# Kernel optimization log

Hardware: AMD Instinct MI355X
Metric: run time of the kernel (lower is better)

## Reference

```python
import jax, jax.numpy as jnp
import numpy as np

N_ITER = 50  # bisection iterations (matches entmax_bisect default)


def entmax_bisect(x, alpha):
    """alpha-entmax via bisection along axis=1. x: [B, L, 1], alpha: [1] (>1)."""
    a_m1 = alpha - 1.0
    inv = 1.0 / a_m1
    xs = x * a_m1
    d = x.shape[1]
    max_val = jnp.max(xs, axis=1, keepdims=True)
    tau_lo = max_val - 1.0
    tau_hi = max_val - (1.0 / d) ** a_m1
    f_lo = jnp.sum(jnp.maximum(xs - tau_lo, 0.0) ** inv, axis=1, keepdims=True) - 1.0

    def body(i, carry):
        tau_lo, dm = carry
        dm = dm * 0.5
        tau_m = tau_lo + dm
        f_m = jnp.sum(jnp.maximum(xs - tau_m, 0.0) ** inv, axis=1, keepdims=True) - 1.0
        tau_lo = jnp.where(f_m * f_lo >= 0.0, tau_m, tau_lo)
        return (tau_lo, dm)

    tau_lo, dm = jax.lax.fori_loop(0, N_ITER, body, (tau_lo, tau_hi - tau_lo))
    p = jnp.maximum(xs - (tau_lo + 0.5 * dm), 0.0) ** inv
    return p / jnp.sum(p, axis=1, keepdims=True)


def setup_inputs() -> dict:
    key = jax.random.key(0)
    ks = jax.random.split(key, 8)
    B, L, E2, D = 256, 512, 512, 256  # E2 = emb_size * 2
    C_target = jax.random.normal(ks[0], (B, E2), jnp.float32)
    C = jax.random.normal(ks[1], (B, L, E2), jnp.float32)
    X = jax.random.normal(ks[2], (B, E2, D), jnp.float32)
    alpha = jnp.array([1.5], jnp.float32)  # entmax-1.5
    mask = jax.random.randint(ks[3], (B, L), 0, 2, jnp.int32).at[:, 0].set(1)
    s = 1.0 / np.sqrt(E2)
    Wg1 = jax.random.uniform(ks[4], (E2, E2), jnp.float32, -s, s)
    Wg2 = jax.random.uniform(ks[5], (E2, E2), jnp.float32, -s, s)
    Wg0 = jax.random.uniform(ks[6], (E2, 1), jnp.float32, -s, s)
    bias_alpha = jax.random.normal(ks[7], (E2,), jnp.float32) * 0.02
    return dict(C_target=C_target, C=C, X=X, alpha=alpha, mask=mask,
                Wg1=Wg1, Wg2=Wg2, Wg0=Wg0, bias_alpha=bias_alpha)


def reference(C_target, C, X, alpha, mask, Wg1, Wg2, Wg0, bias_alpha):
    q = C_target[:, None, :]                               # [B, 1, 2E]
    h = jax.nn.relu(C @ Wg1 + q @ Wg2 + bias_alpha)        # [B, L, 2E]
    score = h @ Wg0                                        # [B, L, 1]
    score = jnp.where(mask[..., None] == 0, -1e30, score)  # mask -> -inf
    p = entmax_bisect(score, alpha)                        # sparse attn over L
    attn = jnp.swapaxes(p, 1, 2) @ C                       # [B, 1, 2E]
    out = jnp.sum(attn @ X, axis=1)                        # [B, D]
    return out
```

## Files before the change

kernel.cpp:

```cpp
#include <hip/hip_runtime.h>
#include <hip/hip_bf16.h>

typedef __bf16 bf16_t;
typedef bf16_t bf16x8 __attribute__((ext_vector_type(8)));
typedef float f32x4 __attribute__((ext_vector_type(4)));

__global__ void k_wg1t(const float* __restrict__ Wg1, bf16_t* __restrict__ Wg1T) {
    __shared__ float tile[32][33];
    const int k0 = blockIdx.x * 32;
    const int e0 = blockIdx.y * 32;
    const int tx = threadIdx.x;
    const int ty = threadIdx.y;
    #pragma unroll
    for (int i = 0; i < 32; i += 8)
        tile[ty + i][tx] = Wg1[(k0 + ty + i) * 512 + e0 + tx];
    __syncthreads();
    #pragma unroll
    for (int i = 0; i < 32; i += 8)
        Wg1T[(e0 + ty + i) * 512 + k0 + tx] = (bf16_t)tile[tx][ty + i];
}

__global__ __launch_bounds__(256) void k_gate(const float* __restrict__ Ct,
                                              const float* __restrict__ Wg2,
                                              const float* __restrict__ bias,
                                              float* __restrict__ g) {
    __shared__ float q[512];
    const int b = blockIdx.x;
    const int t = threadIdx.x;
    q[t]       = Ct[b * 512 + t];
    q[t + 256] = Ct[b * 512 + t + 256];
    __syncthreads();
    const int e = (blockIdx.y << 8) + t;
    float acc = bias[e];
    #pragma unroll 8
    for (int k = 0; k < 512; ++k)
        acc = fmaf(q[k], Wg2[k * 512 + e], acc);
    g[b * 512 + e] = acc;
}

__global__ __launch_bounds__(256, 2) void k_score(const float* __restrict__ C,
                                                  const bf16_t* __restrict__ Wg1T,
                                                  const float* __restrict__ g,
                                                  const float* __restrict__ Wg0,
                                                  const int* __restrict__ mask,
                                                  float* __restrict__ score) {
    __shared__ bf16_t As[64 * 32];
    __shared__ bf16_t Bs[512 * 32];
    __shared__ float  sred[4][64];

    const int t    = threadIdx.x;
    const int lane = t & 63;
    const int wave = t >> 6;
    const int quad = lane >> 4;
    const int l15  = lane & 15;
    const int row0 = blockIdx.x * 64;
    const int b    = row0 >> 9;

    f32x4 acc[4][8] = {};

    for (int kc = 0; kc < 512; kc += 32) {
        __syncthreads();
        #pragma unroll
        for (int i = 0; i < 8; ++i) {
            const int f  = i * 256 + t;
            const int r  = f >> 2;
            const int c8 = (f & 3) << 3;
            __builtin_amdgcn_global_load_lds(
                (const __attribute__((address_space(1))) void*)(Wg1T + r * 512 + kc + c8),
                (__attribute__((address_space(3))) void*)(Bs + f * 8), 16, 0, 0);
        }
        #pragma unroll
        for (int i = 0; i < 2; ++i) {
            const int f  = i * 256 + t;
            const int r  = f >> 3;
            const int c4 = (f & 7) << 2;
            const float4 v = *reinterpret_cast<const float4*>(
                &C[(size_t)(row0 + r) * 512 + kc + c4]);
            union { bf16_t h[4]; uint2 u; } pk;
            pk.h[0] = (bf16_t)v.x; pk.h[1] = (bf16_t)v.y;
            pk.h[2] = (bf16_t)v.z; pk.h[3] = (bf16_t)v.w;
            *reinterpret_cast<uint2*>(&As[r * 32 + c4]) = pk.u;
        }
        __syncthreads();
        bf16x8 afr[4], bfr[8];
        #pragma unroll
        for (int mi = 0; mi < 4; ++mi)
            afr[mi] = *reinterpret_cast<const bf16x8*>(
                &As[(mi * 16 + l15) * 32 + quad * 8]);
        #pragma unroll
        for (int ni = 0; ni < 8; ++ni)
            bfr[ni] = *reinterpret_cast<const bf16x8*>(
                &Bs[(wave * 128 + ni * 16 + l15) * 32 + quad * 8]);
        #pragma unroll
        for (int mi = 0; mi < 4; ++mi)
            #pragma unroll
            for (int ni = 0; ni < 8; ++ni)
                acc[mi][ni] = __builtin_amdgcn_mfma_f32_16x16x32_bf16(
                    afr[mi], bfr[ni], acc[mi][ni], 0, 0, 0);
    }

    float rsum[16];
    #pragma unroll
    for (int i = 0; i < 16; ++i) rsum[i] = 0.f;
    #pragma unroll
    for (int ni = 0; ni < 8; ++ni) {
        const int n  = wave * 128 + ni * 16 + l15;
        const float gv = g[(b << 9) + n];
        const float w0 = Wg0[n];
        #pragma unroll
        for (int mi = 0; mi < 4; ++mi)
            #pragma unroll
            for (int r = 0; r < 4; ++r) {
                float u = fmaxf(acc[mi][ni][r] + gv, 0.f);
                rsum[mi * 4 + r] = fmaf(u, w0, rsum[mi * 4 + r]);
            }
    }
    #pragma unroll
    for (int i = 0; i < 16; ++i) {
        float v = rsum[i];
        v += __shfl_xor(v, 1);
        v += __shfl_xor(v, 2);
        v += __shfl_xor(v, 4);
        v += __shfl_xor(v, 8);
        rsum[i] = v;
    }
    if (l15 == 0) {
        #pragma unroll
        for (int mi = 0; mi < 4; ++mi)
            #pragma unroll
            for (int r = 0; r < 4; ++r)
                sred[wave][mi * 16 + quad * 4 + r] = rsum[mi * 4 + r];
    }
    __syncthreads();
    if (t < 64) {
        const float sc = sred[0][t] + sred[1][t] + sred[2][t] + sred[3][t];
        const int grow = row0 + t;
        score[grow] = (mask[grow] == 0) ? -1e30f : sc;
    }
}

__global__ __launch_bounds__(256) void k_entmax(const float* __restrict__ score,
                                                const float* __restrict__ alpha,
                                                float* __restrict__ p) {
    const int wave = threadIdx.x >> 6;
    const int lane = threadIdx.x & 63;
    const int b    = (blockIdx.x << 2) + wave;
    const float am1 = alpha[0] - 1.0f;
    const float inv = 1.0f / am1;
    const bool  sq  = fabsf(inv - 2.0f) < 1e-6f;

    const float* sb = score + (b << 9);
    float x[8];
    {
        const float4 v0 = *reinterpret_cast<const float4*>(sb + lane * 8);
        const float4 v1 = *reinterpret_cast<const float4*>(sb + lane * 8 + 4);
        x[0] = v0.x * am1; x[1] = v0.y * am1; x[2] = v0.z * am1; x[3] = v0.w * am1;
        x[4] = v1.x * am1; x[5] = v1.y * am1; x[6] = v1.z * am1; x[7] = v1.w * am1;
    }
    float m = x[0];
    #pragma unroll
    for (int j = 1; j < 8; ++j) m = fmaxf(m, x[j]);
    #pragma unroll
    for (int s = 1; s < 64; s <<= 1) m = fmaxf(m, __shfl_xor(m, s));

    float tau_lo = m - 1.0f;
    float dm = (m - powf(1.0f / 512.0f, am1)) - tau_lo;

    float f_lo;
    {
        float s = 0.f;
        #pragma unroll
        for (int j = 0; j < 8; ++j) {
            const float u = fmaxf(x[j] - tau_lo, 0.f);
            s += sq ? u * u : powf(u, inv);
        }
        #pragma unroll
        for (int sh = 1; sh < 64; sh <<= 1) s += __shfl_xor(s, sh);
        f_lo = s - 1.0f;
    }
    for (int it = 0; it < 50; ++it) {
        dm *= 0.5f;
        const float tau_m = tau_lo + dm;
        float s = 0.f;
        #pragma unroll
        for (int j = 0; j < 8; ++j) {
            const float u = fmaxf(x[j] - tau_m, 0.f);
            s += sq ? u * u : powf(u, inv);
        }
        #pragma unroll
        for (int sh = 1; sh < 64; sh <<= 1) s += __shfl_xor(s, sh);
        if ((s - 1.0f) * f_lo >= 0.f) tau_lo = tau_m;
    }
    const float tau = tau_lo + 0.5f * dm;
    float pj[8];
    float Z = 0.f;
    #pragma unroll
    for (int j = 0; j < 8; ++j) {
        const float u = fmaxf(x[j] - tau, 0.f);
        pj[j] = sq ? u * u : powf(u, inv);
        Z += pj[j];
    }
    #pragma unroll
    for (int sh = 1; sh < 64; sh <<= 1) Z += __shfl_xor(Z, sh);
    const float rz = 1.0f / Z;
    float4 o0, o1;
    o0.x = pj[0] * rz; o0.y = pj[1] * rz; o0.z = pj[2] * rz; o0.w = pj[3] * rz;
    o1.x = pj[4] * rz; o1.y = pj[5] * rz; o1.z = pj[6] * rz; o1.w = pj[7] * rz;
    *reinterpret_cast<float4*>(p + (b << 9) + lane * 8)     = o0;
    *reinterpret_cast<float4*>(p + (b << 9) + lane * 8 + 4) = o1;
}

__global__ __launch_bounds__(256) void k_attn(const float* __restrict__ p,
                                              const float* __restrict__ C,
                                              float* __restrict__ part) {
    __shared__ float pv_s[128];
    const int b  = blockIdx.x;
    const int ch = blockIdx.y;
    const int t  = threadIdx.x;
    const float* Cb = C + (size_t)b * 512 * 512 + (size_t)ch * 128 * 512;
    const float* pb = p + (b << 9) + (ch << 7);
    if (t < 128) pv_s[t] = pb[t];
    __syncthreads();
    float a0 = 0.f, a1 = 0.f;
    for (int l = 0; l < 128; ++l) {
        const float pv = pv_s[l];
        if (pv != 0.f) {
            a0 = fmaf(pv, Cb[(size_t)l * 512 + t], a0);
            a1 = fmaf(pv, Cb[(size_t)l * 512 + t + 256], a1);
        }
    }
    float* pp = part + (size_t)((b << 2) + ch) * 512;
    pp[t]       = a0;
    pp[t + 256] = a1;
}

__global__ __launch_bounds__(256) void k_out(const float* __restrict__ part,
                                             const float* __restrict__ X,
                                             float* __restrict__ out) {
    __shared__ float as_[128];
    const int b  = blockIdx.x;
    const int ec = blockIdx.y;
    const int t  = threadIdx.x;
    if (t < 128) {
        const int e = (ec << 7) + t;
        const float* pp = part + (size_t)(b << 2) * 512;
        as_[t] = pp[e] + pp[512 + e] + pp[1024 + e] + pp[1536 + e];
    }
    __syncthreads();
    const float* Xb = X + (size_t)b * 512 * 256 + (size_t)(ec << 7) * 256;
    float acc = 0.f;
    #pragma unroll 4
    for (int e = 0; e < 128; ++e)
        acc = fmaf(as_[e], Xb[e * 256 + t], acc);
    atomicAdd(&out[(b << 8) + t], acc);
}

extern "C" void kernel_launch(void* const* d_in, const int* in_sizes, int n_in,
                              void* d_out, int out_size, void* d_ws, size_t ws_size,
                              hipStream_t stream) {
    const float* C_target = (const float*)d_in[0];
    const float* C        = (const float*)d_in[1];
    const float* X        = (const float*)d_in[2];
    const float* alpha    = (const float*)d_in[3];
    const int*   mask     = (const int*)  d_in[4];
    const float* Wg1      = (const float*)d_in[5];
    const float* Wg2      = (const float*)d_in[6];
    const float* Wg0      = (const float*)d_in[7];
    const float* bias     = (const float*)d_in[8];
    float* out = (float*)d_out;

    char* ws = (char*)d_ws;
    bf16_t* wg1t  = (bf16_t*)(ws);
    float*  g     = (float*)(ws + (512u << 10));
    float*  score = (float*)(ws + (1024u << 10));
    float*  p     = (float*)(ws + (1536u << 10));
    float*  part  = (float*)(ws + (2048u << 10));

    k_wg1t  <<<dim3(16, 16), dim3(32, 8), 0, stream>>>(Wg1, wg1t);
    k_gate  <<<dim3(256, 2), 256, 0, stream>>>(C_target, Wg2, bias, g);
    k_score <<<2048, 256, 0, stream>>>(C, wg1t, g, Wg0, mask, score);
    k_entmax<<<64, 256, 0, stream>>>(score, alpha, p);
    k_attn  <<<dim3(256, 4), 256, 0, stream>>>(p, C, part);
    hipMemsetAsync(d_out, 0, (size_t)out_size * sizeof(float), stream);
    k_out   <<<dim3(256, 4), 256, 0, stream>>>(part, X, out);
}
```

Baseline: 595.5 us.

## Restructure score GEMM: stage C in swizzled LDS, stream Wg1T via registers

The score kernel now converts a 64x256 chunk of C to bf16 in swizzled LDS (two phases over K) instead of looping over 16 small K-chunks. Wg1T is no longer staged through LDS: each wave loads its B fragments straight from global/L2 with register double-buffering. This cuts the number of block barriers and avoids LDS bank conflicts, at the cost of more register pressure and repeated global reads of Wg1T across blocks. Separately, entmax launches one 64-thread block per batch row instead of four rows per block, and the k_out loop unroll is raised to 8.

```diff
diff --git a/kernel.cpp b/kernel.cpp
--- a/kernel.cpp
+++ b/kernel.cpp
@@ -44,8 +44,7 @@
                                                   const float* __restrict__ Wg0,
                                                   const int* __restrict__ mask,
                                                   float* __restrict__ score) {
-    __shared__ bf16_t As[64 * 32];
-    __shared__ bf16_t Bs[512 * 32];
+    __shared__ bf16_t As[64 * 256];
     __shared__ float  sred[4][64];
 
     const int t    = threadIdx.x;
@@ -55,48 +54,61 @@
     const int l15  = lane & 15;
     const int row0 = blockIdx.x * 64;
     const int b    = row0 >> 9;
+    const int nb   = wave * 128;
 
     f32x4 acc[4][8] = {};
 
-    for (int kc = 0; kc < 512; kc += 32) {
+    #pragma unroll
+    for (int ph = 0; ph < 2; ++ph) {
+        const int k0 = ph << 8;
         __syncthreads();
         #pragma unroll
-        for (int i = 0; i < 8; ++i) {
-            const int f  = i * 256 + t;
-            const int r  = f >> 2;
-            const int c8 = (f & 3) << 3;
-            __builtin_amdgcn_global_load_lds(
-                (const __attribute__((address_space(1))) void*)(Wg1T + r * 512 + kc + c8),
-                (__attribute__((address_space(3))) void*)(Bs + f * 8), 16, 0, 0);
-        }
-        #pragma unroll
-        for (int i = 0; i < 2; ++i) {
-            const int f  = i * 256 + t;
-            const int r  = f >> 3;
-            const int c4 = (f & 7) << 2;
+        for (int i = 0; i < 16; ++i) {
+            const int s  = i * 256 + t;
+            const int r  = s >> 6;
+            const int c4 = (s & 63) << 2;
             const float4 v = *reinterpret_cast<const float4*>(
-                &C[(size_t)(row0 + r) * 512 + kc + c4]);
+                &C[(size_t)(row0 + r) * 512 + k0 + c4]);
             union { bf16_t h[4]; uint2 u; } pk;
             pk.h[0] = (bf16_t)v.x; pk.h[1] = (bf16_t)v.y;
             pk.h[2] = (bf16_t)v.z; pk.h[3] = (bf16_t)v.w;
-            *reinterpret_cast<uint2*>(&As[r * 32 + c4]) = pk.u;
+            const int col = ((((c4 >> 3) ^ (r & 31)) << 3) | (c4 & 7));
+            *reinterpret_cast<uint2*>(&As[r * 256 + col]) = pk.u;
         }
         __syncthreads();
-        bf16x8 afr[4], bfr[8];
-        #pragma unroll
-        for (int mi = 0; mi < 4; ++mi)
-            afr[mi] = *reinterpret_cast<const bf16x8*>(
-                &As[(mi * 16 + l15) * 32 + quad * 8]);
+        bf16x8 bcur[8];
         #pragma unroll
         for (int ni = 0; ni < 8; ++ni)
-            bfr[ni] = *reinterpret_cast<const bf16x8*>(
-                &Bs[(wave * 128 + ni * 16 + l15) * 32 + quad * 8]);
-        #pragma unroll
-        for (int mi = 0; mi < 4; ++mi)
-            #pragma unroll
-            for (int ni = 0; ni < 8; ++ni)
-                acc[mi][ni] = __builtin_amdgcn_mfma_f32_16x16x32_bf16(
-                    afr[mi], bfr[ni], acc[mi][ni], 0, 0, 0);
+            bcur[ni] = *reinterpret_cast<const bf16x8*>(
+                &Wg1T[(size_t)(nb + ni * 16 + l15) * 512 + k0 + quad * 8]);
+        #pragma unroll
+        for (int ki = 0; ki < 8; ++ki) {
+            bf16x8 bnxt[8];
+            if (ki < 7) {
+                const int kq = k0 + ((ki + 1) << 5) + quad * 8;
+                #pragma unroll
+                for (int ni = 0; ni < 8; ++ni)
+                    bnxt[ni] = *reinterpret_cast<const bf16x8*>(
+                        &Wg1T[(size_t)(nb + ni * 16 + l15) * 512 + kq]);
+            }
+            bf16x8 afr[4];
+            #pragma unroll
+            for (int mi = 0; mi < 4; ++mi) {
+                const int row  = mi * 16 + l15;
+                const int gidx = ((ki << 2) | quad) ^ (row & 31);
+                afr[mi] = *reinterpret_cast<const bf16x8*>(&As[row * 256 + gidx * 8]);
+            }
+            #pragma unroll
+            for (int mi = 0; mi < 4; ++mi)
+                #pragma unroll
+                for (int ni = 0; ni < 8; ++ni)
+                    acc[mi][ni] = __builtin_amdgcn_mfma_f32_16x16x32_bf16(
+                        afr[mi], bcur[ni], acc[mi][ni], 0, 0, 0);
+            if (ki < 7) {
+                #pragma unroll
+                for (int ni = 0; ni < 8; ++ni) bcur[ni] = bnxt[ni];
+            }
+        }
     }
 
     float rsum[16];
@@ -104,7 +116,7 @@
     for (int i = 0; i < 16; ++i) rsum[i] = 0.f;
     #pragma unroll
     for (int ni = 0; ni < 8; ++ni) {
-        const int n  = wave * 128 + ni * 16 + l15;
+        const int n  = nb + ni * 16 + l15;
         const float gv = g[(b << 9) + n];
         const float w0 = Wg0[n];
         #pragma unroll
@@ -139,12 +151,11 @@
     }
 }
 
-__global__ __launch_bounds__(256) void k_entmax(const float* __restrict__ score,
-                                                const float* __restrict__ alpha,
-                                                float* __restrict__ p) {
-    const int wave = threadIdx.x >> 6;
-    const int lane = threadIdx.x & 63;
-    const int b    = (blockIdx.x << 2) + wave;
+__global__ __launch_bounds__(64) void k_entmax(const float* __restrict__ score,
+                                               const float* __restrict__ alpha,
+                                               float* __restrict__ p) {
+    const int lane = threadIdx.x;
+    const int b    = blockIdx.x;
     const float am1 = alpha[0] - 1.0f;
     const float inv = 1.0f / am1;
     const bool  sq  = fabsf(inv - 2.0f) < 1e-6f;
@@ -249,7 +260,7 @@
     __syncthreads();
     const float* Xb = X + (size_t)b * 512 * 256 + (size_t)(ec << 7) * 256;
     float acc = 0.f;
-    #pragma unroll 4
+    #pragma unroll 8
     for (int e = 0; e < 128; ++e)
         acc = fmaf(as_[e], Xb[e * 256 + t], acc);
     atomicAdd(&out[(b << 8) + t], acc);
@@ -279,7 +290,7 @@
     k_wg1t  <<<dim3(16, 16), dim3(32, 8), 0, stream>>>(Wg1, wg1t);
     k_gate  <<<dim3(256, 2), 256, 0, stream>>>(C_target, Wg2, bias, g);
     k_score <<<2048, 256, 0, stream>>>(C, wg1t, g, Wg0, mask, score);
-    k_entmax<<<64, 256, 0, stream>>>(score, alpha, p);
+    k_entmax<<<256, 64, 0, stream>>>(score, alpha, p);
     k_attn  <<<dim3(256, 4), 256, 0, stream>>>(p, C, part);
     hipMemsetAsync(d_out, 0, (size_t)out_size * sizeof(float), stream);
     k_out   <<<dim3(256, 4), 256, 0, stream>>>(part, X, out);
```

New measurement: 652.7 us. +9.6%, slower.
